# Optimization experiments

Measured on AMD Instinct MI355X. Metric: run time of the kernel, lower is better.

The kernel has to match this reference:

```python
import jax, jax.numpy as jnp
import numpy as np

B, T, D, V = 32, 2048, 256, 2048  # batch, time, embed_dim, num_codebooks


def setup_inputs() -> dict:
    key = jax.random.key(0)
    k1, k2 = jax.random.split(key)
    z = jax.random.normal(k1, (B, T, D), dtype=jnp.float32)
    codebook_weight = jax.random.normal(k2, (V, D), dtype=jnp.float32)
    return {"z": z, "codebook_weight": codebook_weight}


def reference(z, codebook_weight):
    # e = codebook.embedding.weight.clone().detach()
    e = jax.lax.stop_gradient(codebook_weight)            # (V, D)
    zf = z.reshape(-1, e.shape[1])                        # (N, D), N = B*T
    # squared euclidean distances via GEMM expansion
    d = (jnp.sum(zf * zf, axis=1, keepdims=True)
         + jnp.sum(e * e, axis=1)
         - 2.0 * zf @ e.T)                                # (N, V)
    idx = jnp.argmin(d, axis=1)                           # (N,)
    # one-hot matmul with e is mathematically a row gather of e
    z_q = jnp.take(e, idx, axis=0).reshape(z.shape)       # (B, T, D)
    commitment_loss = jnp.mean((z - jax.lax.stop_gradient(z_q)) ** 2)
    z_q_st = z + jax.lax.stop_gradient(z_q - z)           # straight-through
    encoding_indices = idx.reshape(z.shape[0], z.shape[1])  # (B, T)
    hist = jnp.bincount(idx, length=V).astype(jnp.float32)
    codebook_prob = hist / (hist.sum() + 1e-8)
    return commitment_loss, z_q_st, encoding_indices, codebook_prob
```

## Files before the change

### kernel.cpp

```cpp
#include <hip/hip_runtime.h>

#define NROWS 65536
#define DIM   256
#define VCB   2048
#define DELTA 0.25f

typedef _Float16 f16;
typedef _Float16 f16x8 __attribute__((ext_vector_type(8)));
typedef float    f32x4 __attribute__((ext_vector_type(4)));


__device__ __forceinline__ void async16(void* lds, const void* g) {
  __builtin_amdgcn_global_load_lds(
      (const __attribute__((address_space(1))) void*)g,
      (__attribute__((address_space(3))) void*)lds, 16, 0, 0);
}

__global__ __launch_bounds__(256) void convert_kernel(
    const float4* __restrict__ src, short4* __restrict__ dhi,
    short4* __restrict__ dlo, int n4) {
  int stride = gridDim.x * 256;
  for (int i = blockIdx.x * 256 + threadIdx.x; i < n4; i += stride) {
    float4 v = src[i];
    union { f16 h[4]; short4 s; } H, L;
    H.h[0] = (f16)v.x; H.h[1] = (f16)v.y; H.h[2] = (f16)v.z; H.h[3] = (f16)v.w;
    L.h[0] = (f16)(v.x - (float)H.h[0]);
    L.h[1] = (f16)(v.y - (float)H.h[1]);
    L.h[2] = (f16)(v.z - (float)H.h[2]);
    L.h[3] = (f16)(v.w - (float)H.h[3]);
    dhi[i] = H.s; dlo[i] = L.s;
  }
}

__global__ __launch_bounds__(256) void prep_kernel(
    const float* __restrict__ e, float* __restrict__ enorm,
    unsigned int* __restrict__ hist, double* __restrict__ loss_part,
    int* __restrict__ flag_cnt) {
  int tid = threadIdx.x;
  int gt = blockIdx.x * 256 + tid;
  if (gt == 0) flag_cnt[0] = 0;
  if (gt < VCB) hist[gt] = 0u;
  if (gt < 256) loss_part[gt] = 0.0;
  int wid  = gt >> 6;
  int lane = tid & 63;
  if (wid < VCB) {
    const float4* row = (const float4*)(e + (size_t)wid * DIM);
    float4 v = row[lane];
    float s = v.x*v.x + v.y*v.y + v.z*v.z + v.w*v.w;
    #pragma unroll
    for (int off = 32; off; off >>= 1) s += __shfl_xor(s, off);
    if (lane == 0) enorm[wid] = s;
  }
}

__global__ __launch_bounds__(512) void pass1_kernel(
    const float* __restrict__ z, const f16* __restrict__ eh,
    const float* __restrict__ enorm,
    int* __restrict__ idx_out, unsigned int* __restrict__ hist,
    double* __restrict__ loss_part,
    int* __restrict__ flag_cnt, int* __restrict__ flag_list) {
  __shared__ f16 ldsA[8][2048];
  __shared__ f16 ldsB[3][8192];

  const int tid  = threadIdx.x;
  const int wid  = tid >> 6;
  const int lane = tid & 63;
  const int wr   = wid >> 2;
  const int wc   = wid & 3;
  const int lrow = lane & 15;
  const int lq   = lane >> 4;
  const int rbase = blockIdx.x * 64;

  auto stageB = [&](int b, int ss, int kt) {
    #pragma unroll
    for (int i = 0; i < 2; ++i) {
      int col   = wid * 32 + i * 16 + (lane >> 2);
      int chunk = lane & 3;
      int gk    = chunk ^ ((col >> 1) & 3);
      size_t goff = (size_t)(ss * 256 + col) * DIM + (kt << 5) + (gk << 3);
      async16(&ldsB[b][0] + col * 32 + chunk * 8, eh + goff);
    }
  };

  {
    const int row = tid >> 3;
    const int q   = tid & 7;
    const float* zrow = z + (size_t)(rbase + row) * DIM + q * 32;
    const int sw = (row >> 1) & 3;
    float zs = 0.f;
    #pragma unroll
    for (int f = 0; f < 8; ++f) {
      float4 v = *(const float4*)(zrow + f * 4);
      int chunk  = f >> 1;
      int within = (f & 1) * 8;
      int addr = q * 4096 + row * 64 + ((chunk ^ sw) << 4) + within;
      union { f16 h[4]; short4 s4; } H;
      H.h[0] = (f16)v.x; H.h[1] = (f16)v.y; H.h[2] = (f16)v.z; H.h[3] = (f16)v.w;
      *(short4*)((char*)ldsA + addr) = H.s4;
      zs += v.x*v.x + v.y*v.y + v.z*v.z + v.w*v.w;
    }
    #pragma unroll
    for (int off = 32; off; off >>= 1) zs += __shfl_xor(zs, off);
    if (lane == 0) atomicAdd(&loss_part[blockIdx.x & 255], (double)zs);
  }
  stageB(0, 0, 0);
  asm volatile("s_waitcnt vmcnt(0)" ::: "memory");
  __syncthreads();

  float m1[2][4], m2v[2][4];
  int   i1[2][4];
  #pragma unroll
  for (int m = 0; m < 2; ++m)
    #pragma unroll
    for (int r = 0; r < 4; ++r) { m1[m][r] = 3.4e38f; m2v[m][r] = 3.4e38f; i1[m][r] = 0; }

  const int cchunk = lq ^ ((lrow >> 1) & 3);

  int pb = 0;
  for (int ss = 0; ss < 8; ++ss) {
    f32x4 acc[2][4];
    #pragma unroll
    for (int m = 0; m < 2; ++m)
      #pragma unroll
      for (int n = 0; n < 4; ++n) {
        f32x4 zz = {0.f, 0.f, 0.f, 0.f};
        acc[m][n] = zz;
      }

    for (int kt = 0; kt < 8; ++kt) {
      int nkt = kt + 1, nss = ss;
      if (nkt == 8) { nkt = 0; ++nss; if (nss == 8) nss = 0; }
      int nxt = pb + 1; if (nxt == 3) nxt = 0;
      stageB(nxt, nss, nkt);
      asm volatile("s_waitcnt vmcnt(2)" ::: "memory");
      asm volatile("s_barrier" ::: "memory");
      __builtin_amdgcn_sched_barrier(0);

      const char* abase = (const char*)ldsA + kt * 4096;
      f16x8 ah[2];
      #pragma unroll
      for (int m = 0; m < 2; ++m) {
        int row = wr * 32 + m * 16 + lrow;
        ah[m] = *(const f16x8*)(abase + row * 64 + cchunk * 16);
      }
      const char* bbase = (const char*)&ldsB[pb][0];
      #pragma unroll
      for (int n = 0; n < 4; ++n) {
        int col = wc * 64 + n * 16 + lrow;
        f16x8 bh = *(const f16x8*)(bbase + col * 64 + cchunk * 16);
        #pragma unroll
        for (int m = 0; m < 2; ++m)
          acc[m][n] = __builtin_amdgcn_mfma_f32_16x16x32_f16(ah[m], bh, acc[m][n], 0, 0, 0);
      }
      pb = nxt;
    }

    #pragma unroll
    for (int n = 0; n < 4; ++n) {
      int j = ss * 256 + wc * 64 + n * 16 + lrow;
      float en = enorm[j];
      #pragma unroll
      for (int m = 0; m < 2; ++m)
        #pragma unroll
        for (int r = 0; r < 4; ++r) {
          float s = fmaf(-2.f, acc[m][n][r], en);
          if (s < m1[m][r]) { m2v[m][r] = m1[m][r]; m1[m][r] = s; i1[m][r] = j; }
          else if (s < m2v[m][r]) m2v[m][r] = s;
        }
    }
  }
  asm volatile("s_waitcnt vmcnt(0)" ::: "memory");

  #pragma unroll
  for (int off = 1; off < 16; off <<= 1) {
    #pragma unroll
    for (int m = 0; m < 2; ++m)
      #pragma unroll
      for (int r = 0; r < 4; ++r) {
        float o1 = __shfl_xor(m1[m][r], off);
        int   oi = __shfl_xor(i1[m][r], off);
        float o2 = __shfl_xor(m2v[m][r], off);
        float nm2 = fminf(fminf(m2v[m][r], o2), fmaxf(m1[m][r], o1));
        if (o1 < m1[m][r] || (o1 == m1[m][r] && oi < i1[m][r])) {
          m1[m][r] = o1; i1[m][r] = oi;
        }
        m2v[m][r] = nm2;
      }
  }

  __syncthreads();
  float* sx1 = (float*)&ldsB[0][0];
  float* sx2 = sx1 + 3 * 2 * 32;
  int*   sxi = (int*)(sx2 + 3 * 2 * 32);
  if (wc != 0 && lrow == 0) {
    #pragma unroll
    for (int m = 0; m < 2; ++m)
      #pragma unroll
      for (int r = 0; r < 4; ++r) {
        int li = m * 16 + lq * 4 + r;
        int ix = ((wc - 1) * 2 + wr) * 32 + li;
        sx1[ix] = m1[m][r];
        sx2[ix] = m2v[m][r];
        sxi[ix] = i1[m][r];
      }
  }
  __syncthreads();
  if (wc == 0 && lrow == 0) {
    float lsum = 0.f;
    #pragma unroll
    for (int m = 0; m < 2; ++m)
      #pragma unroll
      for (int r = 0; r < 4; ++r) {
        int li = m * 16 + lq * 4 + r;
        float v  = m1[m][r];
        int   bi = i1[m][r];
        float v2 = m2v[m][r];
        #pragma unroll
        for (int g = 0; g < 3; ++g) {
          int ix = (g * 2 + wr) * 32 + li;
          float ov = sx1[ix];
          float o2 = sx2[ix];
          int   oi = sxi[ix];
          float nm2 = fminf(fminf(v2, o2), fmaxf(v, ov));
          if (ov < v || (ov == v && oi < bi)) { v = ov; bi = oi; }
          v2 = nm2;
        }
        int row = rbase + wr * 32 + li;
        if (v2 - v <= DELTA) {
          int p = atomicAdd(flag_cnt, 1);
          flag_list[p] = row;
        } else {
          idx_out[row] = bi;
          atomicAdd(&hist[bi], 1u);
          lsum += v;
        }
      }
    lsum += __shfl_xor(lsum, 16);
    lsum += __shfl_xor(lsum, 32);
    if (lane == 0) atomicAdd(&loss_part[blockIdx.x & 255], (double)lsum);
  }
}

__global__ __launch_bounds__(512) void pass2_kernel(
    const float* __restrict__ z,
    const f16* __restrict__ eh, const f16* __restrict__ el,
    const float* __restrict__ enorm,
    const int* __restrict__ flag_cnt, const int* __restrict__ flag_list,
    float* __restrict__ pval, int* __restrict__ pidx) {
  __shared__ f16 ldsA[8][8192];
  __shared__ f16 ldsB[2][8192];

  const int tid  = threadIdx.x;
  const int wid  = tid >> 6;
  const int lane = tid & 63;
  const int wr   = wid >> 2;
  const int wc   = wid & 3;
  const int lrow = lane & 15;
  const int lq   = lane >> 4;
  const int srow = tid >> 2;
  const int scol = tid & 3;
  const int skoff = ((scol ^ ((srow >> 1) & 3)) << 3);
  const int cchunk = lq ^ ((lrow >> 1) & 3);
  const int cnt = *flag_cnt;

  auto stageB = [&](int b, int vcol, int kt) {
    size_t off = (size_t)(vcol + srow) * DIM + (kt << 5) + skoff;
    async16(&ldsB[b][0]    + tid * 8, eh + off);
    async16(&ldsB[b][4096] + tid * 8, el + off);
  };

  for (int job = blockIdx.x; ; job += gridDim.x) {
    int chunk = job >> 4, cb = job & 15;
    int base = chunk * 128;
    if (base >= cnt) break;
    int nrows = cnt - base; if (nrows > 128) nrows = 128;

    __syncthreads();

    {
      const int row = tid >> 2;
      const int q   = tid & 3;
      int grow = flag_list[base + (row < nrows ? row : 0)];
      const float* zrow = z + (size_t)grow * DIM + q * 64;
      const int sw = (row >> 1) & 3;
      #pragma unroll
      for (int f = 0; f < 16; ++f) {
        float4 v = *(const float4*)(zrow + f * 4);
        int col4   = q * 64 + f * 4;
        int kt     = col4 >> 5;
        int ko     = col4 & 31;
        int chunk2 = ko >> 3;
        int within = (ko & 7) * 2;
        int addr = kt * 16384 + row * 64 + ((chunk2 ^ sw) << 4) + within;
        union { f16 h[4]; short4 s4; } H, L;
        H.h[0] = (f16)v.x; H.h[1] = (f16)v.y; H.h[2] = (f16)v.z; H.h[3] = (f16)v.w;
        L.h[0] = (f16)(v.x - (float)H.h[0]);
        L.h[1] = (f16)(v.y - (float)H.h[1]);
        L.h[2] = (f16)(v.z - (float)H.h[2]);
        L.h[3] = (f16)(v.w - (float)H.h[3]);
        *(short4*)((char*)ldsA + addr)        = H.s4;
        *(short4*)((char*)ldsA + addr + 8192) = L.s4;
      }
    }
    int pb = 0;
    stageB(0, cb * 128, 0);
    asm volatile("s_waitcnt vmcnt(0)" ::: "memory");
    __syncthreads();

    float minv[4][4];
    int   mini[4][4];
    #pragma unroll
    for (int m = 0; m < 4; ++m)
      #pragma unroll
      for (int r = 0; r < 4; ++r) { minv[m][r] = 3.4e38f; mini[m][r] = 0; }

    f32x4 acc[4][2];
    #pragma unroll
    for (int m = 0; m < 4; ++m)
      #pragma unroll
      for (int n = 0; n < 2; ++n) {
        f32x4 zz = {0.f, 0.f, 0.f, 0.f};
        acc[m][n] = zz;
      }

    for (int kt = 0; kt < 8; ++kt) {
      if (kt < 7) {
        stageB(pb ^ 1, cb * 128, kt + 1);
        asm volatile("s_waitcnt vmcnt(2)" ::: "memory");
      } else {
        asm volatile("s_waitcnt vmcnt(0)" ::: "memory");
      }
      asm volatile("s_barrier" ::: "memory");
      __builtin_amdgcn_sched_barrier(0);

      const char* abase = (const char*)&ldsA[kt][0];
      f16x8 ah[4], al[4];
      #pragma unroll
      for (int m = 0; m < 4; ++m) {
        int row = wr * 64 + m * 16 + lrow;
        int off = row * 64 + cchunk * 16;
        ah[m] = *(const f16x8*)(abase + off);
        al[m] = *(const f16x8*)(abase + 8192 + off);
      }
      const char* bbase = (const char*)&ldsB[pb][0];
      #pragma unroll
      for (int n = 0; n < 2; ++n) {
        int col = wc * 32 + n * 16 + lrow;
        int off = col * 64 + cchunk * 16;
        f16x8 bh = *(const f16x8*)(bbase + off);
        f16x8 bl = *(const f16x8*)(bbase + 8192 + off);
        #pragma unroll
        for (int m = 0; m < 4; ++m) {
          acc[m][n] = __builtin_amdgcn_mfma_f32_16x16x32_f16(ah[m], bh, acc[m][n], 0, 0, 0);
          acc[m][n] = __builtin_amdgcn_mfma_f32_16x16x32_f16(ah[m], bl, acc[m][n], 0, 0, 0);
          acc[m][n] = __builtin_amdgcn_mfma_f32_16x16x32_f16(al[m], bh, acc[m][n], 0, 0, 0);
        }
      }
      __builtin_amdgcn_sched_barrier(0);
      asm volatile("s_barrier" ::: "memory");
      pb ^= 1;
    }

    #pragma unroll
    for (int n = 0; n < 2; ++n) {
      int j = cb * 128 + wc * 32 + n * 16 + lrow;
      float en = enorm[j];
      #pragma unroll
      for (int m = 0; m < 4; ++m)
        #pragma unroll
        for (int r = 0; r < 4; ++r) {
          float s = fmaf(-2.f, acc[m][n][r], en);
          if (s < minv[m][r]) { minv[m][r] = s; mini[m][r] = j; }
        }
    }

    #pragma unroll
    for (int off = 1; off < 16; off <<= 1) {
      #pragma unroll
      for (int m = 0; m < 4; ++m)
        #pragma unroll
        for (int r = 0; r < 4; ++r) {
          float ov = __shfl_xor(minv[m][r], off);
          int   oi = __shfl_xor(mini[m][r], off);
          if (ov < minv[m][r] || (ov == minv[m][r] && oi < mini[m][r])) {
            minv[m][r] = ov; mini[m][r] = oi;
          }
        }
    }

    __syncthreads();
    float* sxv = (float*)&ldsB[0][0];
    int*   sxi2 = (int*)(sxv + 3 * 2 * 64);
    if (wc != 0 && lrow == 0) {
      #pragma unroll
      for (int m = 0; m < 4; ++m)
        #pragma unroll
        for (int r = 0; r < 4; ++r) {
          int li = m * 16 + lq * 4 + r;
          int ix = ((wc - 1) * 2 + wr) * 64 + li;
          sxv[ix] = minv[m][r];
          sxi2[ix] = mini[m][r];
        }
    }
    __syncthreads();
    if (wc == 0 && lrow == 0) {
      #pragma unroll
      for (int m = 0; m < 4; ++m)
        #pragma unroll
        for (int r = 0; r < 4; ++r) {
          int li = m * 16 + lq * 4 + r;
          float v  = minv[m][r];
          int   bi = mini[m][r];
          #pragma unroll
          for (int g = 0; g < 3; ++g) {
            int ix = (g * 2 + wr) * 64 + li;
            float ov = sxv[ix];
            int   oi = sxi2[ix];
            if (ov < v || (ov == v && oi < bi)) { v = ov; bi = oi; }
          }
          int i = wr * 64 + li;
          if (i < nrows) {
            int fi = base + i;
            pval[fi * 16 + cb] = v;
            pidx[fi * 16 + cb] = bi;
          }
        }
    }
  }
}

__global__ __launch_bounds__(256) void pass2m_kernel(
    const int* __restrict__ flag_cnt, const int* __restrict__ flag_list,
    const float* __restrict__ pval, const int* __restrict__ pidx,
    int* __restrict__ idx_out, unsigned int* __restrict__ hist,
    double* __restrict__ loss_part) {
  int cnt = *flag_cnt;
  int t = blockIdx.x * 256 + threadIdx.x;
  int stride = gridDim.x * 256;
  for (int fi = t; fi < cnt; fi += stride) {
    float m = 3.4e38f; int bi = 0;
    #pragma unroll
    for (int cb = 0; cb < 16; ++cb) {
      float v = pval[fi * 16 + cb];
      int  ix = pidx[fi * 16 + cb];
      if (v < m || (v == m && ix < bi)) { m = v; bi = ix; }
    }
    int row = flag_list[fi];
    idx_out[row] = bi;
    atomicAdd(&hist[bi], 1u);
    atomicAdd(&loss_part[fi & 255], (double)m);
  }
}

__global__ __launch_bounds__(256) void gather_kernel(
    const float* __restrict__ e, const int* __restrict__ idx,
    float* __restrict__ zq_out, float* __restrict__ idxf_out) {
  int tid  = threadIdx.x;
  int w    = tid >> 6;
  int lane = tid & 63;
  int n    = blockIdx.x * 4 + w;

  int ci = idx[n];
  const float4* er = (const float4*)(e + (size_t)ci * DIM);
  ((float4*)(zq_out + (size_t)n * DIM))[lane] = er[lane];
  if (lane == 0) idxf_out[n] = (float)ci;
}

__global__ __launch_bounds__(256) void finalize_kernel(
    const unsigned int* __restrict__ hist, const double* __restrict__ loss_part,
    float* __restrict__ out) {
  __shared__ double lsh[4];
  __shared__ float  hsh[4];
  __shared__ float  denom_sh;
  int tid = threadIdx.x, lane = tid & 63, w = tid >> 6;

  float hs = 0.f;
  for (int j = tid; j < VCB; j += 256) hs += (float)hist[j];
  double ls = loss_part[tid];
  #pragma unroll
  for (int off = 32; off; off >>= 1) {
    hs += __shfl_xor(hs, off);
    ls += __shfl_xor(ls, off);
  }
  if (lane == 0) { lsh[w] = ls; hsh[w] = hs; }
  __syncthreads();
  if (tid == 0) {
    double lt = lsh[0] + lsh[1] + lsh[2] + lsh[3];
    float  ht = hsh[0] + hsh[1] + hsh[2] + hsh[3];
    out[0] = (float)(lt / (double)((size_t)NROWS * DIM));
    denom_sh = ht + 1e-8f;
  }
  __syncthreads();
  float denom = denom_sh;
  float* prob = out + 1 + (size_t)NROWS * DIM + NROWS;
  for (int j = tid; j < VCB; j += 256) prob[j] = (float)hist[j] / denom;
}

extern "C" void kernel_launch(void* const* d_in, const int* in_sizes, int n_in,
                              void* d_out, int out_size, void* d_ws, size_t ws_size,
                              hipStream_t stream) {
  (void)in_sizes; (void)n_in; (void)out_size; (void)ws_size;
  const float* z = (const float*)d_in[0];
  const float* e = (const float*)d_in[1];
  float* out = (float*)d_out;
  char*  ws  = (char*)d_ws;

  int*          idx       = (int*)ws;
  unsigned int* hist      = (unsigned int*)(ws + 262144);
  double*       loss_part = (double*)(ws + 270336);
  float*        enorm     = (float*)(ws + 272384);
  int*          flag_cnt  = (int*)(ws + 280576);
  f16*          e_hi      = (f16*)(ws + 524288);
  f16*          e_lo      = (f16*)(ws + 1572864);

  float* pval      = out + 32;
  int*   pidx      = (int*)(out + 32 + 1048576);
  int*   flag_list = (int*)(out + 32 + 2097152);

  float* out_zq  = out + 1;
  float* out_idx = out + 1 + (size_t)NROWS * DIM;

  convert_kernel<<<128, 256, 0, stream>>>(
      (const float4*)e, (short4*)e_hi, (short4*)e_lo, VCB * DIM / 4);
  prep_kernel<<<512, 256, 0, stream>>>(e, enorm, hist, loss_part, flag_cnt);
  pass1_kernel<<<NROWS / 64, 512, 0, stream>>>(
      z, e_hi, enorm, idx, hist, loss_part, flag_cnt, flag_list);
  pass2_kernel<<<512, 512, 0, stream>>>(
      z, e_hi, e_lo, enorm, flag_cnt, flag_list, pval, pidx);
  pass2m_kernel<<<64, 256, 0, stream>>>(
      flag_cnt, flag_list, pval, pidx, idx, hist, loss_part);
  gather_kernel<<<NROWS / 4, 256, 0, stream>>>(e, idx, out_zq, out_idx);
  finalize_kernel<<<1, 256, 0, stream>>>(hist, loss_part, out);
}
```

Baseline: 211.3 us.

## Stage codebook in half-K double buffers to cut barriers per sweep

```diff
diff --git a/kernel.cpp b/kernel.cpp
--- a/kernel.cpp
+++ b/kernel.cpp
@@ -60,7 +60,7 @@
     double* __restrict__ loss_part,
     int* __restrict__ flag_cnt, int* __restrict__ flag_list) {
   __shared__ f16 ldsA[8][2048];
-  __shared__ f16 ldsB[3][8192];
+  __shared__ f16 ldsB[2][32768];
 
   const int tid  = threadIdx.x;
   const int wid  = tid >> 6;
@@ -71,14 +71,17 @@
   const int lq   = lane >> 4;
   const int rbase = blockIdx.x * 64;
 
-  auto stageB = [&](int b, int ss, int kt) {
-    #pragma unroll
-    for (int i = 0; i < 2; ++i) {
-      int col   = wid * 32 + i * 16 + (lane >> 2);
-      int chunk = lane & 3;
-      int gk    = chunk ^ ((col >> 1) & 3);
-      size_t goff = (size_t)(ss * 256 + col) * DIM + (kt << 5) + (gk << 3);
-      async16(&ldsB[b][0] + col * 32 + chunk * 8, eh + goff);
+  auto stageB = [&](int b, int ss, int kh) {
+    #pragma unroll
+    for (int ks = 0; ks < 4; ++ks) {
+      #pragma unroll
+      for (int i = 0; i < 2; ++i) {
+        int col   = wid * 32 + i * 16 + (lane >> 2);
+        int chunk = lane & 3;
+        int gk    = chunk ^ ((col >> 1) & 3);
+        size_t goff = (size_t)(ss * 256 + col) * DIM + kh * 128 + ks * 32 + (gk << 3);
+        async16(&ldsB[b][ks * 8192] + col * 32 + chunk * 8, eh + goff);
+      }
     }
   };
 
@@ -103,9 +106,8 @@
     for (int off = 32; off; off >>= 1) zs += __shfl_xor(zs, off);
     if (lane == 0) atomicAdd(&loss_part[blockIdx.x & 255], (double)zs);
   }
+  __syncthreads();
   stageB(0, 0, 0);
-  asm volatile("s_waitcnt vmcnt(0)" ::: "memory");
-  __syncthreads();
 
   float m1[2][4], m2v[2][4];
   int   i1[2][4];
@@ -116,34 +118,35 @@
 
   const int cchunk = lq ^ ((lrow >> 1) & 3);
 
-  int pb = 0;
-  for (int ss = 0; ss < 8; ++ss) {
-    f32x4 acc[2][4];
-    #pragma unroll
-    for (int m = 0; m < 2; ++m)
-      #pragma unroll
-      for (int n = 0; n < 4; ++n) {
-        f32x4 zz = {0.f, 0.f, 0.f, 0.f};
-        acc[m][n] = zz;
-      }
-
-    for (int kt = 0; kt < 8; ++kt) {
-      int nkt = kt + 1, nss = ss;
-      if (nkt == 8) { nkt = 0; ++nss; if (nss == 8) nss = 0; }
-      int nxt = pb + 1; if (nxt == 3) nxt = 0;
-      stageB(nxt, nss, nkt);
-      asm volatile("s_waitcnt vmcnt(2)" ::: "memory");
-      asm volatile("s_barrier" ::: "memory");
-      __builtin_amdgcn_sched_barrier(0);
-
-      const char* abase = (const char*)ldsA + kt * 4096;
+  f32x4 acc[2][4];
+  for (int p = 0; p < 16; ++p) {
+    const int ss = p >> 1, kh = p & 1;
+    const int pb = p & 1;
+    if (kh == 0) {
+      #pragma unroll
+      for (int m = 0; m < 2; ++m)
+        #pragma unroll
+        for (int n = 0; n < 4; ++n) {
+          f32x4 zz = {0.f, 0.f, 0.f, 0.f};
+          acc[m][n] = zz;
+        }
+    }
+
+    asm volatile("s_waitcnt vmcnt(0)" ::: "memory");
+    asm volatile("s_barrier" ::: "memory");
+    __builtin_amdgcn_sched_barrier(0);
+    if (p + 1 < 16) stageB(pb ^ 1, (p + 1) >> 1, (p + 1) & 1);
+
+    #pragma unroll
+    for (int ks = 0; ks < 4; ++ks) {
+      const char* abase = (const char*)ldsA + (kh * 4 + ks) * 4096;
       f16x8 ah[2];
       #pragma unroll
       for (int m = 0; m < 2; ++m) {
         int row = wr * 32 + m * 16 + lrow;
         ah[m] = *(const f16x8*)(abase + row * 64 + cchunk * 16);
       }
-      const char* bbase = (const char*)&ldsB[pb][0];
+      const char* bbase = (const char*)&ldsB[pb][ks * 8192];
       #pragma unroll
       for (int n = 0; n < 4; ++n) {
         int col = wc * 64 + n * 16 + lrow;
@@ -152,24 +155,24 @@
         for (int m = 0; m < 2; ++m)
           acc[m][n] = __builtin_amdgcn_mfma_f32_16x16x32_f16(ah[m], bh, acc[m][n], 0, 0, 0);
       }
-      pb = nxt;
-    }
-
-    #pragma unroll
-    for (int n = 0; n < 4; ++n) {
-      int j = ss * 256 + wc * 64 + n * 16 + lrow;
-      float en = enorm[j];
-      #pragma unroll
-      for (int m = 0; m < 2; ++m)
-        #pragma unroll
-        for (int r = 0; r < 4; ++r) {
-          float s = fmaf(-2.f, acc[m][n][r], en);
-          if (s < m1[m][r]) { m2v[m][r] = m1[m][r]; m1[m][r] = s; i1[m][r] = j; }
-          else if (s < m2v[m][r]) m2v[m][r] = s;
-        }
-    }
-  }
-  asm volatile("s_waitcnt vmcnt(0)" ::: "memory");
+    }
+
+    if (kh == 1) {
+      #pragma unroll
+      for (int n = 0; n < 4; ++n) {
+        int j = ss * 256 + wc * 64 + n * 16 + lrow;
+        float en = enorm[j];
+        #pragma unroll
+        for (int m = 0; m < 2; ++m)
+          #pragma unroll
+          for (int r = 0; r < 4; ++r) {
+            float s = fmaf(-2.f, acc[m][n][r], en);
+            if (s < m1[m][r]) { m2v[m][r] = m1[m][r]; m1[m][r] = s; i1[m][r] = j; }
+            else if (s < m2v[m][r]) m2v[m][r] = s;
+          }
+      }
+    }
+  }
 
   #pragma unroll
   for (int off = 1; off < 16; off <<= 1) {
```

Result: slower. 246.7 us (+16.7%).
